# Kernel tuning notes

Measured on AMD Instinct MI355X. Metric: run time of the kernel, lower is better.

The kernel has to match this reference:

```python
import jax, jax.numpy as jnp
import numpy as np

B, T, N, F = 4, 24, 1024, 96
H, HD = 3, 32      # spatial GATConv: 3 heads, head-dim 32 (averaged -> 32 per branch, 3 branches -> 96)
GH, GHD = 4, 24    # GroupedGAT: 4 heads concatenated -> 96
E = 8192           # edges per graph


def setup_inputs() -> dict:
    key = jax.random.key(0)
    ks = jax.random.split(key, 24)
    s_in = 1.0 / np.sqrt(F)
    def gat_params(k):
        k1, k2, k3, k4 = jax.random.split(k, 4)
        return (jax.random.normal(k1, (F, H * HD), jnp.float32) * s_in,
                jax.random.normal(k2, (H, HD), jnp.float32) * 0.1,
                jax.random.normal(k3, (H, HD), jnp.float32) * 0.1,
                jax.random.normal(k4, (H, HD), jnp.float32) * 0.02)
    W_d, al_d, ar_d, b_d = gat_params(ks[3])
    W_m, al_m, ar_m, b_m = gat_params(ks[4])
    W_s, al_s, ar_s, b_s = gat_params(ks[5])
    inp = {
        "input": jax.random.normal(ks[0], (B, T, N, F), jnp.float32),
        "spatial_embedding": jax.random.normal(ks[1], (B, T, N, F), jnp.float32),
        "temporal_embedding": jax.random.normal(ks[2], (B, T, N, F), jnp.float32),
        "src_d": jax.random.randint(ks[6], (E,), 0, N, jnp.int32),
        "dst_d": (jnp.arange(E) % N).astype(jnp.int32),
        "src_m": jax.random.randint(ks[7], (E,), 0, N, jnp.int32),
        "dst_m": (jnp.arange(E) % N).astype(jnp.int32),
        "src_s": jax.random.randint(ks[8], (E,), 0, N, jnp.int32),
        "dst_s": (jnp.arange(E) % N).astype(jnp.int32),
        "W_d": W_d, "al_d": al_d, "ar_d": ar_d, "b_d": b_d,
        "W_m": W_m, "al_m": al_m, "ar_m": ar_m, "b_m": b_m,
        "W_s": W_s, "al_s": al_s, "ar_s": ar_s, "b_s": b_s,
        "Wg": jax.random.normal(ks[9], (F, GH * GHD), jnp.float32) * s_in,
        "agl": jax.random.normal(ks[10], (GH, GHD), jnp.float32) * 0.1,
        "agr": jax.random.normal(ks[11], (GH, GHD), jnp.float32) * 0.1,
        "Wf": jax.random.normal(ks[12], (2 * F, F), jnp.float32) * (1.0 / np.sqrt(2 * F)),
        "bf": jnp.zeros((F,), jnp.float32),
    }
    return inp


def _gat(x, src, dst, W, al, ar, b):
    # x: (N, K, F) node features with K = T*B batched feature slots
    K = x.shape[1]
    h = (x @ W).reshape(N, K, H, HD)                       # (N,K,H,HD)
    el = (h * al).sum(-1)                                  # (N,K,H)
    er = (h * ar).sum(-1)
    e = jax.nn.leaky_relu(el[src] + er[dst], 0.2)          # (E,K,H)
    emax = jax.ops.segment_max(e, dst, num_segments=N)
    emax = jnp.where(jnp.isfinite(emax), emax, 0.0)
    ex = jnp.exp(e - emax[dst])
    denom = jax.ops.segment_sum(ex, dst, num_segments=N)
    alpha = ex / (denom[dst] + 1e-9)                       # edge softmax over incoming edges
    out = jax.ops.segment_sum(h[src] * alpha[..., None], dst, num_segments=N)
    return (out + b).mean(2)                               # average heads -> (N,K,HD)


def reference(input, spatial_embedding, temporal_embedding,
              src_d, dst_d, src_m, dst_m, src_s, dst_s,
              W_d, al_d, ar_d, b_d, W_m, al_m, ar_m, b_m, W_s, al_s, ar_s, b_s,
              Wg, agl, agr, Wf, bf):
    # ---------------- SpatialBlock ----------------
    residual_s = input                                     # input_dim == output_dim
    x_in = input + spatial_embedding
    # torch: input.transpose(0,2).reshape(N,-1,F) -> slot order is (t,b)
    x = jnp.transpose(x_in, (2, 1, 0, 3)).reshape(N, T * B, F)
    xd = _gat(x, src_d, dst_d, W_d, al_d, ar_d, b_d)
    xm = _gat(x, src_m, dst_m, W_m, al_m, ar_m, b_m)
    xs = _gat(x, src_s, dst_s, W_s, al_s, ar_s, b_s)
    x_attn = jnp.concatenate([xd, xm, xs], axis=-1)        # (N, T*B, 3*HD=F)
    # torch: transpose(0,1).reshape(batch,T,N,-1)  (keeps original (t,b) slot order quirk)
    x_attn = jnp.transpose(x_attn, (1, 0, 2)).reshape(B, T, N, F)
    cov0 = spatial_embedding[:, 0]                         # (B,N,F)
    attn_S = jax.nn.softmax(cov0 @ jnp.swapaxes(cov0, 1, 2), axis=2)  # (B,N,N)
    # NOTE: embedding_x branch in SpatialBlock is dead code (out is overwritten); skipped.
    spatial = residual_s + x_attn

    # ---------------- TemporalBlock ----------------
    residual_t = input
    xt = jnp.swapaxes(input, 1, 2).reshape(B * N, T, F)    # (B*N, T, F), index k=b*N+n
    # GroupedGAT: dense multi-head GAT over the T=period_num time steps
    hg = (xt @ Wg).reshape(B * N, T, GH, GHD)
    elg = (hg * agl).sum(-1)                               # (BN,T,GH)
    erg = (hg * agr).sum(-1)
    eg = jax.nn.leaky_relu(elg[:, :, None, :] + erg[:, None, :, :], 0.2)  # (BN,Ti,Tj,GH)
    alphag = jax.nn.softmax(eg, axis=2)
    xg = jnp.einsum('kijh,kjhd->kihd', alphag, hg).reshape(B * N, T, GH * GHD)
    covT = temporal_embedding[:, :, 0]                     # (B,T,F)
    attn_T = jax.nn.softmax(covT @ jnp.swapaxes(covT, 1, 2), axis=1)      # softmax over dim=1 as in torch
    # torch: attn.repeat(N,1,1) paired with x of batch index b*N+n -> uses attn[(b*N+n) % B]
    idx = (jnp.arange(B * N) % B)
    emb = jnp.einsum('kij,kjf->kif', attn_T[idx], xt)      # (BN,T,F)
    xg = xg * jax.nn.sigmoid(emb)
    xg = jnp.swapaxes(xg.reshape(B, N, T, F), 1, 2)        # (B,T,N,F)
    temporal = residual_t + xg

    # ---------------- Fusion ----------------
    z = jax.nn.sigmoid(jnp.concatenate([spatial, temporal], axis=-1) @ Wf + bf)
    out = z * spatial + (1.0 - z) * temporal + input
    return out, attn_S
```

## Files before the change

### kernel.cpp

```cpp
#include <hip/hip_runtime.h>
#include <hip/hip_bf16.h>

typedef long long i64;
typedef __attribute__((ext_vector_type(8))) short short8b;
typedef __attribute__((ext_vector_type(4))) short short4b;
typedef __attribute__((ext_vector_type(4))) float f32x4;

union U8 { short8b v; ushort s[8]; };
union U4 { short4b v; ushort s[4]; };

static __device__ __forceinline__ float bs2f(ushort u) {
    union { unsigned int i; float f; } x; x.i = ((unsigned int)u) << 16; return x.f;
}
static __device__ __forceinline__ ushort f2bs(float f) {
    __hip_bfloat16 h = __float2bfloat16(f);
    return *reinterpret_cast<ushort*>(&h);
}
static __device__ __forceinline__ void mfma_bf16(f32x4& acc, short8b a, short8b b) {
    asm volatile("v_mfma_f32_16x16x32_bf16 %0, %1, %2, %0" : "+v"(acc) : "v"(a), "v"(b));
}
static __device__ __forceinline__ void mfma_fence() {
    asm volatile("s_nop 7\n\ts_nop 7\n\ts_nop 7");
}


__global__ __launch_bounds__(256) void prep_weights_kernel(
        const float* __restrict__ Wd, const float* __restrict__ Wm,
        const float* __restrict__ Ws, const float* __restrict__ Wg,
        const float* __restrict__ Wf,
        const float* __restrict__ ald, const float* __restrict__ ard,
        const float* __restrict__ alm, const float* __restrict__ arm,
        const float* __restrict__ als, const float* __restrict__ ars,
        const float* __restrict__ agl, const float* __restrict__ agr,
        ushort* __restrict__ wtab) {
    int idx = blockIdx.x * 256 + threadIdx.x;
    if (idx >= 61440) return;
    if (idx < 43008) {
        int w = idx / 10752, rem = idx - w * 10752;
        int c = rem / 96, k = rem - c * 96;
        float v;
        if (w < 3) {
            const float* W = (w == 0) ? Wd : (w == 1) ? Wm : Ws;
            if (c < 96) {
                v = W[k * 96 + c];
            } else {
                int j = c - 96, h = j >> 1;
                const float* a = (j & 1) ? ((w == 0) ? ard : (w == 1) ? arm : ars)
                                         : ((w == 0) ? ald : (w == 1) ? alm : als);
                v = 0.f;
                for (int d = 0; d < 32; ++d) v += W[k * 96 + h * 32 + d] * a[h * 32 + d];
            }
        } else {
            if (c < 96) {
                v = Wg[k * 96 + c];
            } else {
                int j = c - 96, g = j & 3;
                const float* a = (j >> 2) ? agr : agl;
                v = 0.f;
                for (int d = 0; d < 24; ++d) v += Wg[k * 96 + g * 24 + d] * a[g * 24 + d];
            }
        }
        wtab[w * 10752 + c * 96 + k] = f2bs(v);
    } else {
        int rem = idx - 43008;
        int c = rem / 192, k = rem - c * 192;
        wtab[43008 + c * 192 + k] = f2bs(Wf[k * 96 + c]);
    }
}

__global__ __launch_bounds__(256) void build_x_kernel(const float* __restrict__ inp,
                                                      const float* __restrict__ spat,
                                                      ushort* __restrict__ x) {
    int i4 = blockIdx.x * 256 + threadIdx.x;
    int q = i4 % 24;
    int r = i4 / 24;
    int n = r & 1023, bt = r >> 10;
    int t = bt % 24, b = bt / 24;
    int k = t * 4 + b;
    float4 a = ((const float4*)inp)[i4];
    float4 s = ((const float4*)spat)[i4];
    U4 u;
    u.s[0] = f2bs(a.x + s.x); u.s[1] = f2bs(a.y + s.y);
    u.s[2] = f2bs(a.z + s.z); u.s[3] = f2bs(a.w + s.w);
    *(short4b*)&x[((i64)((k << 10) | n)) * 96 + q * 4] = u.v;
}

__global__ __launch_bounds__(256) void gemm96_mfma_kernel(const ushort* __restrict__ X,
                                                          const ushort* __restrict__ wt,
                                                          ushort* __restrict__ Ho,
                                                          float* __restrict__ el,
                                                          float* __restrict__ er) {
    __shared__ ushort Xs[128 * 104];
    __shared__ ushort Wt[112 * 104];
    int tid = threadIdx.x;
    i64 row0 = (i64)blockIdx.x * 128;
    for (int i = tid; i < 1344; i += 256) {
        int c = i / 12, kg = i - c * 12;
        *(short8b*)&Wt[c * 104 + kg * 8] = *(const short8b*)&wt[c * 96 + kg * 8];
    }
    for (int i = tid; i < 1536; i += 256) {
        int r = i / 12, q = i - r * 12;
        *(short8b*)&Xs[r * 104 + q * 8] = *(const short8b*)&X[(row0 + r) * 96 + q * 8];
    }
    __syncthreads();
    int wid = tid >> 6, lane = tid & 63;
    int lr = lane & 15, lk = lane >> 4;
    f32x4 acc[2][7];
#pragma unroll
    for (int m = 0; m < 2; ++m)
#pragma unroll
        for (int c = 0; c < 7; ++c) acc[m][c] = (f32x4){0.f, 0.f, 0.f, 0.f};
    const ushort* xa = &Xs[(wid * 32 + lr) * 104 + lk * 8];
    const ushort* wb = &Wt[lr * 104 + lk * 8];
#pragma unroll
    for (int ks = 0; ks < 3; ++ks) {
        short8b a0 = *(const short8b*)(xa + ks * 32);
        short8b a1 = *(const short8b*)(xa + 16 * 104 + ks * 32);
#pragma unroll
        for (int c = 0; c < 7; ++c) {
            short8b b = *(const short8b*)(wb + c * 16 * 104 + ks * 32);
            mfma_bf16(acc[0][c], a0, b);
            mfma_bf16(acc[1][c], a1, b);
        }
    }
    mfma_fence();
#pragma unroll
    for (int m = 0; m < 2; ++m) {
#pragma unroll
        for (int c = 0; c < 6; ++c)
#pragma unroll
            for (int r = 0; r < 4; ++r) {
                i64 row = row0 + wid * 32 + m * 16 + lk * 4 + r;
                Ho[row * 96 + c * 16 + lr] = f2bs(acc[m][c][r]);
            }
        if (lr < 6) {
            float* dst = (lr & 1) ? er : el;
            int h = lr >> 1;
#pragma unroll
            for (int r = 0; r < 4; ++r) {
                i64 row = row0 + wid * 32 + m * 16 + lk * 4 + r;
                dst[row * 3 + h] = acc[m][6][r];
            }
        }
    }
}

__global__ __launch_bounds__(256) void gemm96_hg_mfma_kernel(const float* __restrict__ inp,
                                                             const ushort* __restrict__ wt,
                                                             ushort* __restrict__ Ho,
                                                             float* __restrict__ elg,
                                                             float* __restrict__ erg) {
    __shared__ ushort Xs[128 * 104];
    __shared__ ushort Wt[112 * 104];
    int tid = threadIdx.x;
    i64 row0 = (i64)blockIdx.x * 128;
    for (int i = tid; i < 1344; i += 256) {
        int c = i / 12, kg = i - c * 12;
        *(short8b*)&Wt[c * 104 + kg * 8] = *(const short8b*)&wt[c * 96 + kg * 8];
    }
    for (int i = tid; i < 3072; i += 256) {
        int r = i / 24, q = i - r * 24;
        int row = (int)row0 + r;
        int kk = row / 24, t = row - kk * 24;
        int b = kk >> 10, n = kk & 1023;
        float4 v = ((const float4*)inp)[((i64)(((b * 24 + t) << 10) | n)) * 24 + q];
        U4 u;
        u.s[0] = f2bs(v.x); u.s[1] = f2bs(v.y); u.s[2] = f2bs(v.z); u.s[3] = f2bs(v.w);
        *(short4b*)&Xs[r * 104 + q * 4] = u.v;
    }
    __syncthreads();
    int wid = tid >> 6, lane = tid & 63;
    int lr = lane & 15, lk = lane >> 4;
    f32x4 acc[2][7];
#pragma unroll
    for (int m = 0; m < 2; ++m)
#pragma unroll
        for (int c = 0; c < 7; ++c) acc[m][c] = (f32x4){0.f, 0.f, 0.f, 0.f};
    const ushort* xa = &Xs[(wid * 32 + lr) * 104 + lk * 8];
    const ushort* wb = &Wt[lr * 104 + lk * 8];
#pragma unroll
    for (int ks = 0; ks < 3; ++ks) {
        short8b a0 = *(const short8b*)(xa + ks * 32);
        short8b a1 = *(const short8b*)(xa + 16 * 104 + ks * 32);
#pragma unroll
        for (int c = 0; c < 7; ++c) {
            short8b b = *(const short8b*)(wb + c * 16 * 104 + ks * 32);
            mfma_bf16(acc[0][c], a0, b);
            mfma_bf16(acc[1][c], a1, b);
        }
    }
    mfma_fence();
#pragma unroll
    for (int m = 0; m < 2; ++m) {
#pragma unroll
        for (int c = 0; c < 6; ++c)
#pragma unroll
            for (int r = 0; r < 4; ++r) {
                i64 row = row0 + wid * 32 + m * 16 + lk * 4 + r;
                Ho[row * 96 + c * 16 + lr] = f2bs(acc[m][c][r]);
            }
        if (lr < 8) {
            float* dst = (lr >> 2) ? erg : elg;
            int g = lr & 3;
#pragma unroll
            for (int r = 0; r < 4; ++r) {
                i64 row = row0 + wid * 32 + m * 16 + lk * 4 + r;
                dst[row * 4 + g] = acc[m][6][r];
            }
        }
    }
}

__global__ __launch_bounds__(256) void gat_agg_kernel(const ushort* __restrict__ H2,
                                                      const float* __restrict__ el,
                                                      const float* __restrict__ er,
                                                      const int* __restrict__ src,
                                                      const float* __restrict__ bv,
                                                      ushort* __restrict__ xattn,
                                                      int g) {
    int tid = threadIdx.x;
    int pp = tid >> 3, l8 = tid & 7;
    int p = blockIdx.x * 32 + pp;
    int k = p >> 10, n = p & 1023;
    int d0 = l8 * 4;
    i64 kb = (i64)(k << 10);
    int s_own = src[n + l8 * 1024];
    const float* elp = &el[(kb | s_own) * 3];
    const float* erp = &er[(kb | n) * 3];
    float e[3], m[3];
#pragma unroll
    for (int h = 0; h < 3; ++h) {
        float ev = elp[h] + erp[h];
        e[h] = ev >= 0.f ? ev : 0.2f * ev;
        m[h] = e[h];
    }
#pragma unroll
    for (int mask = 1; mask < 8; mask <<= 1) {
#pragma unroll
        for (int h = 0; h < 3; ++h) m[h] = fmaxf(m[h], __shfl_xor(m[h], mask, 8));
    }
    float pex[3], S[3];
#pragma unroll
    for (int h = 0; h < 3; ++h) { pex[h] = expf(e[h] - m[h]); S[h] = pex[h]; }
#pragma unroll
    for (int mask = 1; mask < 8; mask <<= 1) {
#pragma unroll
        for (int h = 0; h < 3; ++h) S[h] += __shfl_xor(S[h], mask, 8);
    }
    float w[3];
#pragma unroll
    for (int h = 0; h < 3; ++h) w[h] = pex[h] / (S[h] + 1e-9f);
    float acc[4] = {0.f, 0.f, 0.f, 0.f};
#pragma unroll
    for (int j = 0; j < 8; ++j) {
        int sj = __shfl(s_own, j, 8);
        float a0 = __shfl(w[0], j, 8);
        float a1 = __shfl(w[1], j, 8);
        float a2 = __shfl(w[2], j, 8);
        const ushort* hp = &H2[(kb | sj) * 96 + d0];
        U4 h0, h1, h2;
        h0.v = *(const short4b*)&hp[0];
        h1.v = *(const short4b*)&hp[32];
        h2.v = *(const short4b*)&hp[64];
#pragma unroll
        for (int c = 0; c < 4; ++c)
            acc[c] += a0 * bs2f(h0.s[c]) + a1 * bs2f(h1.s[c]) + a2 * bs2f(h2.s[c]);
    }
    float4 b0 = *(const float4*)&bv[d0];
    float4 b1 = *(const float4*)&bv[32 + d0];
    float4 b2 = *(const float4*)&bv[64 + d0];
    float bsum[4] = {b0.x + b1.x + b2.x, b0.y + b1.y + b2.y,
                     b0.z + b1.z + b2.z, b0.w + b1.w + b2.w};
    U4 u;
#pragma unroll
    for (int c = 0; c < 4; ++c) u.s[c] = f2bs((acc[c] + bsum[c]) * (1.f / 3.f));
    *(short4b*)&xattn[(kb | n) * 96 + g * 32 + d0] = u.v;
}

__global__ __launch_bounds__(256) void attn_scores_kernel(const float* __restrict__ spat,
                                                          float* __restrict__ attnS) {
    int bid = blockIdx.x;
    int b = bid >> 8;
    int i0 = ((bid >> 4) & 15) * 64;
    int j0 = (bid & 15) * 64;
    const float* C = spat + (i64)b * 24 * 1024 * 96;
    __shared__ __align__(16) float As[64 * 100];
    __shared__ __align__(16) float Bs[64 * 100];
    int tid = threadIdx.x;
    float4* As4 = (float4*)As;
    float4* Bs4 = (float4*)Bs;
    const float4* Ai = (const float4*)(C + (i64)i0 * 96);
    const float4* Bj = (const float4*)(C + (i64)j0 * 96);
    for (int i = tid; i < 1536; i += 256) {
        int row = i / 24, q = i - row * 24;
        As4[row * 25 + q] = Ai[i];
        Bs4[row * 25 + q] = Bj[i];
    }
    __syncthreads();
    int tj = tid & 15, ti = tid >> 4;
    float acc[4][4];
#pragma unroll
    for (int r = 0; r < 4; ++r)
#pragma unroll
        for (int s = 0; s < 4; ++s) acc[r][s] = 0.f;
    for (int k4 = 0; k4 < 24; ++k4) {
        float4 a[4], bv[4];
#pragma unroll
        for (int r = 0; r < 4; ++r) a[r] = As4[(ti * 4 + r) * 25 + k4];
#pragma unroll
        for (int s = 0; s < 4; ++s) bv[s] = Bs4[(s * 16 + tj) * 25 + k4];
#pragma unroll
        for (int r = 0; r < 4; ++r)
#pragma unroll
            for (int s = 0; s < 4; ++s)
                acc[r][s] += a[r].x * bv[s].x + a[r].y * bv[s].y + a[r].z * bv[s].z + a[r].w * bv[s].w;
    }
#pragma unroll
    for (int r = 0; r < 4; ++r) {
        i64 orow = ((i64)(b << 10) + i0 + ti * 4 + r) * 1024 + j0;
#pragma unroll
        for (int s = 0; s < 4; ++s) attnS[orow + s * 16 + tj] = acc[r][s];
    }
}

__global__ __launch_bounds__(256) void attn_softmax_kernel(float* __restrict__ attnS) {
    i64 base = (i64)blockIdx.x * 1024;
    float4* row4 = (float4*)(attnS + base);
    int tid = threadIdx.x;
    float4 v = row4[tid];
    __shared__ float red[256];
    float m = fmaxf(fmaxf(v.x, v.y), fmaxf(v.z, v.w));
    red[tid] = m;
    __syncthreads();
    for (int st = 128; st > 0; st >>= 1) {
        if (tid < st) red[tid] = fmaxf(red[tid], red[tid + st]);
        __syncthreads();
    }
    m = red[0];
    __syncthreads();
    v.x = expf(v.x - m); v.y = expf(v.y - m); v.z = expf(v.z - m); v.w = expf(v.w - m);
    red[tid] = v.x + v.y + v.z + v.w;
    __syncthreads();
    for (int st = 128; st > 0; st >>= 1) {
        if (tid < st) red[tid] += red[tid + st];
        __syncthreads();
    }
    float inv = 1.f / red[0];
    v.x *= inv; v.y *= inv; v.z *= inv; v.w *= inv;
    row4[tid] = v;
}

__global__ __launch_bounds__(576) void attn_t_kernel(const float* __restrict__ temp,
                                                     float* __restrict__ attnT) {
    int b = blockIdx.x;
    int tid = threadIdx.x;
    __shared__ float cs[24][96];
    __shared__ float M[24][24];
    for (int i = tid; i < 2304; i += 576) {
        int r = i / 96, f = i - r * 96;
        cs[r][f] = temp[((i64)(b * 24 + r)) * 1024 * 96 + f];
    }
    __syncthreads();
    int i = tid / 24, j = tid - i * 24;
    float s = 0.f;
#pragma unroll
    for (int f = 0; f < 96; ++f) s += cs[i][f] * cs[j][f];
    M[i][j] = s;
    __syncthreads();
    float m = -1e30f;
#pragma unroll
    for (int i2 = 0; i2 < 24; ++i2) m = fmaxf(m, M[i2][j]);
    float sum = 0.f;
#pragma unroll
    for (int i2 = 0; i2 < 24; ++i2) sum += expf(M[i2][j] - m);
    attnT[((i64)b * 24 + i) * 24 + j] = expf(M[i][j] - m) / sum;
}

__global__ __launch_bounds__(192) void temporal_kernel(const float* __restrict__ inp,
                                                       const ushort* __restrict__ hg,
                                                       const float* __restrict__ elgb,
                                                       const float* __restrict__ ergb,
                                                       const float* __restrict__ attnT,
                                                       ushort* __restrict__ gated) {
    int kk = blockIdx.x;
    int b = kk >> 10, n = kk & 1023;
    __shared__ __align__(16) ushort hgs[24 * 96];
    __shared__ __align__(16) ushort xs[24 * 96];
    __shared__ __align__(16) float alphaT[4][24][32];
    __shared__ __align__(16) float atT[24][32];
    __shared__ __align__(16) float elg[24][4], erg[24][4];
    int tid = threadIdx.x;
    for (int i = tid; i < 576; i += 192)
        *(short4b*)&hgs[i * 4] = *(const short4b*)&hg[(i64)kk * 2304 + i * 4];
    for (int i = tid; i < 576; i += 192) {
        int r = i / 24, q = i - r * 24;
        float4 v = ((const float4*)inp)[(((i64)(b * 24 + r)) << 10 | n) * 24 + q];
        U4 u;
        u.s[0] = f2bs(v.x); u.s[1] = f2bs(v.y); u.s[2] = f2bs(v.z); u.s[3] = f2bs(v.w);
        *(short4b*)&xs[r * 96 + q * 4] = u.v;
    }
    int ib = kk & 3;
    for (int i = tid; i < 576; i += 192) {
        int ii = i / 24, j = i - ii * 24;
        atT[j][(ii / 3) * 4 + (ii - (ii / 3) * 3)] = attnT[ib * 576 + i];
    }
    for (int i = tid; i < 48; i += 192) {
        int r = i >> 1;
        if (i & 1) *(float4*)&erg[r][0] = ((const float4*)ergb)[(i64)kk * 24 + r];
        else       *(float4*)&elg[r][0] = ((const float4*)elgb)[(i64)kk * 24 + r];
    }
    __syncthreads();
    {
        int i = tid >> 3, g = (tid >> 1) & 3, half = tid & 1;
        int j0 = half * 12;
        float eli = elg[i][g];
        float ev[12];
        float m = -1e30f;
#pragma unroll
        for (int j = 0; j < 12; ++j) {
            float e = eli + erg[j0 + j][g];
            e = e >= 0.f ? e : 0.2f * e;
            ev[j] = e;
            m = fmaxf(m, e);
        }
        m = fmaxf(m, __shfl_xor(m, 1));
        float sum = 0.f;
#pragma unroll
        for (int j = 0; j < 12; ++j) { ev[j] = expf(ev[j] - m); sum += ev[j]; }
        sum += __shfl_xor(sum, 1);
        float inv = 1.f / sum;
        int slot = (i / 3) * 4 + (i - (i / 3) * 3);
#pragma unroll
        for (int j = 0; j < 12; ++j) alphaT[g][j0 + j][slot] = ev[j] * inv;
    }
    __syncthreads();
    int ig = tid / 24, f4 = tid - (tid / 24) * 24;
    int g = f4 / 6;
    float4 xg0 = {0,0,0,0}, xg1 = {0,0,0,0}, xg2 = {0,0,0,0};
    float4 em0 = {0,0,0,0}, em1 = {0,0,0,0}, em2 = {0,0,0,0};
#pragma unroll
    for (int j = 0; j < 24; ++j) {
        U4 uh, ux;
        uh.v = *(const short4b*)&hgs[j * 96 + f4 * 4];
        ux.v = *(const short4b*)&xs[j * 96 + f4 * 4];
        float4 a4 = *(const float4*)&alphaT[g][j][ig * 4];
        float4 w4 = *(const float4*)&atT[j][ig * 4];
        float h0 = bs2f(uh.s[0]), h1 = bs2f(uh.s[1]), h2 = bs2f(uh.s[2]), h3 = bs2f(uh.s[3]);
        float x0 = bs2f(ux.s[0]), x1 = bs2f(ux.s[1]), x2 = bs2f(ux.s[2]), x3 = bs2f(ux.s[3]);
        xg0.x += a4.x * h0; xg0.y += a4.x * h1; xg0.z += a4.x * h2; xg0.w += a4.x * h3;
        xg1.x += a4.y * h0; xg1.y += a4.y * h1; xg1.z += a4.y * h2; xg1.w += a4.y * h3;
        xg2.x += a4.z * h0; xg2.y += a4.z * h1; xg2.z += a4.z * h2; xg2.w += a4.z * h3;
        em0.x += w4.x * x0; em0.y += w4.x * x1; em0.z += w4.x * x2; em0.w += w4.x * x3;
        em1.x += w4.y * x0; em1.y += w4.y * x1; em1.z += w4.y * x2; em1.w += w4.y * x3;
        em2.x += w4.z * x0; em2.y += w4.z * x1; em2.z += w4.z * x2; em2.w += w4.z * x3;
    }
    i64 obase = (i64)kk * 2304 + f4 * 4;
#pragma unroll
    for (int r = 0; r < 3; ++r) {
        float4 xg = (r == 0) ? xg0 : (r == 1) ? xg1 : xg2;
        float4 em = (r == 0) ? em0 : (r == 1) ? em1 : em2;
        U4 o;
        o.s[0] = f2bs(xg.x / (1.f + expf(-em.x)));
        o.s[1] = f2bs(xg.y / (1.f + expf(-em.y)));
        o.s[2] = f2bs(xg.z / (1.f + expf(-em.z)));
        o.s[3] = f2bs(xg.w / (1.f + expf(-em.w)));
        *(short4b*)&gated[obase + (i64)(ig * 3 + r) * 96] = o.v;
    }
}

__global__ __launch_bounds__(256) void fusion_mfma_kernel(const float* __restrict__ inp,
                                                          const ushort* __restrict__ xattn,
                                                          const ushort* __restrict__ gated,
                                                          const ushort* __restrict__ wtf,
                                                          const float* __restrict__ bfv,
                                                          float* __restrict__ outb) {
    __shared__ ushort Xs[64 * 200];
    __shared__ ushort Wt[96 * 200];
    int tid = threadIdx.x;
    i64 row0 = (i64)blockIdx.x * 64;
    for (int i = tid; i < 2304; i += 256) {
        int c = i / 24, kg = i - c * 24;
        *(short8b*)&Wt[c * 200 + kg * 8] = *(const short8b*)&wtf[c * 192 + kg * 8];
    }
    for (int i = tid; i < 768; i += 256) {
        int r = i / 12, q = i - r * 12;
        i64 grow = row0 + r;
        int n = (int)(grow & 1023);
        int bt = (int)(grow >> 10);
        int t = bt % 24, b = bt / 24;
        float4 iv0 = ((const float4*)inp)[grow * 24 + q * 2];
        float4 iv1 = ((const float4*)inp)[grow * 24 + q * 2 + 1];
        U8 xa; xa.v = *(const short8b*)&xattn[grow * 96 + q * 8];
        U8 gd; gd.v = *(const short8b*)&gated[(((i64)((b << 10) | n)) * 24 + t) * 96 + q * 8];
        float ivf[8] = {iv0.x, iv0.y, iv0.z, iv0.w, iv1.x, iv1.y, iv1.z, iv1.w};
        U8 sp, tm;
#pragma unroll
        for (int j = 0; j < 8; ++j) {
            sp.s[j] = f2bs(ivf[j] + bs2f(xa.s[j]));
            tm.s[j] = f2bs(ivf[j] + bs2f(gd.s[j]));
        }
        *(short8b*)&Xs[r * 200 + q * 8] = sp.v;
        *(short8b*)&Xs[r * 200 + 96 + q * 8] = tm.v;
    }
    __syncthreads();
    int wid = tid >> 6, lane = tid & 63;
    int lr = lane & 15, lk = lane >> 4;
    f32x4 acc[6];
#pragma unroll
    for (int c = 0; c < 6; ++c) acc[c] = (f32x4){0.f, 0.f, 0.f, 0.f};
    const ushort* xa = &Xs[(wid * 16 + lr) * 200 + lk * 8];
    const ushort* wb = &Wt[lr * 200 + lk * 8];
#pragma unroll
    for (int ks = 0; ks < 6; ++ks) {
        short8b a = *(const short8b*)(xa + ks * 32);
#pragma unroll
        for (int c = 0; c < 6; ++c) {
            short8b b = *(const short8b*)(wb + c * 16 * 200 + ks * 32);
            mfma_bf16(acc[c], a, b);
        }
    }
    mfma_fence();
#pragma unroll
    for (int c = 0; c < 6; ++c) {
        int col = c * 16 + lr;
        float bfc = bfv[col];
#pragma unroll
        for (int r = 0; r < 4; ++r) {
            int lrow = wid * 16 + lk * 4 + r;
            i64 grow = row0 + lrow;
            float z = 1.f / (1.f + expf(-(acc[c][r] + bfc)));
            float sp = bs2f(Xs[lrow * 200 + col]);
            float tm = bs2f(Xs[lrow * 200 + 96 + col]);
            float iv = inp[grow * 96 + col];
            outb[grow * 96 + col] = z * sp + (1.f - z) * tm + iv;
        }
    }
}

extern "C" void kernel_launch(void* const* d_in, const int* in_sizes, int n_in,
                              void* d_out, int out_size, void* d_ws, size_t ws_size,
                              hipStream_t stream) {
    const float* input = (const float*)d_in[0];
    const float* spat  = (const float*)d_in[1];
    const float* temp  = (const float*)d_in[2];
    const int* src_d = (const int*)d_in[3];
    const int* src_m = (const int*)d_in[5];
    const int* src_s = (const int*)d_in[7];
    const float* W_d  = (const float*)d_in[9];
    const float* al_d = (const float*)d_in[10];
    const float* ar_d = (const float*)d_in[11];
    const float* b_d  = (const float*)d_in[12];
    const float* W_m  = (const float*)d_in[13];
    const float* al_m = (const float*)d_in[14];
    const float* ar_m = (const float*)d_in[15];
    const float* b_m  = (const float*)d_in[16];
    const float* W_s  = (const float*)d_in[17];
    const float* al_s = (const float*)d_in[18];
    const float* ar_s = (const float*)d_in[19];
    const float* b_s  = (const float*)d_in[20];
    const float* Wg   = (const float*)d_in[21];
    const float* agl  = (const float*)d_in[22];
    const float* agr  = (const float*)d_in[23];
    const float* Wf   = (const float*)d_in[24];
    const float* bf_  = (const float*)d_in[25];

    float* outb  = (float*)d_out;
    float* attnS = outb + 9437184;

    float* wsf = (float*)d_ws;
    ushort* xbf      = (ushort*)wsf;
    ushort* hgbf     = xbf;
    ushort* H2bf     = (ushort*)(wsf + 4718592);
    ushort* gatedbf  = H2bf;
    ushort* xattnbf  = (ushort*)(wsf + 9437184);
    float* el    = wsf + 14155776;
    float* er    = el + 294912;
    float* elgb  = wsf + 14155776;
    float* attnT = wsf + 14745600;
    float* ergb  = wsf + 14747904;
    ushort* wtab = (ushort*)(wsf + 15141120);
    ushort* wt_d = wtab;
    ushort* wt_m = wtab + 10752;
    ushort* wt_s = wtab + 21504;
    ushort* wtg  = wtab + 32256;
    ushort* wtf  = wtab + 43008;

    prep_weights_kernel<<<240, 256, 0, stream>>>(W_d, W_m, W_s, Wg, Wf,
                                                 al_d, ar_d, al_m, ar_m, al_s, ar_s,
                                                 agl, agr, wtab);
    build_x_kernel<<<9216, 256, 0, stream>>>(input, spat, xbf);

    const ushort* Wgat[3] = {wt_d, wt_m, wt_s};
    const float* bgat[3] = {b_d, b_m, b_s};
    const int* srcs[3] = {src_d, src_m, src_s};
    for (int g = 0; g < 3; ++g) {
        gemm96_mfma_kernel<<<768, 256, 0, stream>>>(xbf, Wgat[g], H2bf, el, er);
        gat_agg_kernel<<<3072, 256, 0, stream>>>(H2bf, el, er, srcs[g], bgat[g],
                                                 xattnbf, g);
    }

    attn_scores_kernel<<<1024, 256, 0, stream>>>(spat, attnS);
    attn_softmax_kernel<<<4096, 256, 0, stream>>>(attnS);

    gemm96_hg_mfma_kernel<<<768, 256, 0, stream>>>(input, wtg, hgbf, elgb, ergb);
    attn_t_kernel<<<4, 576, 0, stream>>>(temp, attnT);
    temporal_kernel<<<4096, 192, 0, stream>>>(input, hgbf, elgb, ergb, attnT, gatedbf);
    fusion_mfma_kernel<<<1536, 256, 0, stream>>>(input, xattnbf, gatedbf, wtf, bf_, outb);
}
```

Before: 245.1 us.

## Split temporal kernel into sigmoid-embedding and grouped-GAT aggregation kernels

Splits the fused temporal kernel in two. A new 576-thread kernel computes sigmoid(attn_T @ x) in fp32 and writes it as bf16 into the output buffer, used as scratch. The aggregation kernel then only computes the grouped-GAT weighted sum and multiplies by the precomputed sigmoid, with an XOR swizzle on the alpha shared-memory layout to reduce bank conflicts. The goal is lower register and LDS pressure per kernel, bought with an extra 18MB bf16 round trip through global memory and one more launch.

```diff
diff --git a/kernel.cpp b/kernel.cpp
--- a/kernel.cpp
+++ b/kernel.cpp
@@ -376,34 +376,50 @@
     attnT[((i64)b * 24 + i) * 24 + j] = expf(M[i][j] - m) / sum;
 }
 
-__global__ __launch_bounds__(192) void temporal_kernel(const float* __restrict__ inp,
-                                                       const ushort* __restrict__ hg,
-                                                       const float* __restrict__ elgb,
-                                                       const float* __restrict__ ergb,
-                                                       const float* __restrict__ attnT,
-                                                       ushort* __restrict__ gated) {
+__global__ __launch_bounds__(576) void sig_kernel(const float* __restrict__ inp,
+                                                  const float* __restrict__ attnT,
+                                                  ushort* __restrict__ sig) {
     int kk = blockIdx.x;
     int b = kk >> 10, n = kk & 1023;
+    __shared__ __align__(16) float xs[24 * 100];
+    __shared__ float ats[576];
+    int tid = threadIdx.x;
+    {
+        int r = tid / 24, q = tid - (tid / 24) * 24;
+        *(float4*)&xs[r * 100 + q * 4] =
+            ((const float4*)inp)[(((i64)(b * 24 + r)) << 10 | n) * 24 + q];
+        ats[tid] = attnT[(kk & 3) * 576 + tid];
+    }
+    __syncthreads();
+    int i = tid / 24, f4 = tid - (tid / 24) * 24;
+    const float* ap = &ats[i * 24];
+    float4 acc = {0.f, 0.f, 0.f, 0.f};
+#pragma unroll
+    for (int j = 0; j < 24; ++j) {
+        float a = ap[j];
+        float4 v = *(const float4*)&xs[j * 100 + f4 * 4];
+        acc.x += a * v.x; acc.y += a * v.y; acc.z += a * v.z; acc.w += a * v.w;
+    }
+    U4 o;
+    o.s[0] = f2bs(1.f / (1.f + expf(-acc.x)));
+    o.s[1] = f2bs(1.f / (1.f + expf(-acc.y)));
+    o.s[2] = f2bs(1.f / (1.f + expf(-acc.z)));
+    o.s[3] = f2bs(1.f / (1.f + expf(-acc.w)));
+    *(short4b*)&sig[(i64)kk * 2304 + i * 96 + f4 * 4] = o.v;
+}
+
+__global__ __launch_bounds__(192) void xg_kernel(const ushort* __restrict__ hg,
+                                                 const float* __restrict__ elgb,
+                                                 const float* __restrict__ ergb,
+                                                 const ushort* __restrict__ sig,
+                                                 ushort* __restrict__ gated) {
+    int kk = blockIdx.x;
     __shared__ __align__(16) ushort hgs[24 * 96];
-    __shared__ __align__(16) ushort xs[24 * 96];
-    __shared__ __align__(16) float alphaT[4][24][32];
-    __shared__ __align__(16) float atT[24][32];
+    __shared__ __align__(16) float alphaT[4 * 24 * 32];
     __shared__ __align__(16) float elg[24][4], erg[24][4];
     int tid = threadIdx.x;
     for (int i = tid; i < 576; i += 192)
         *(short4b*)&hgs[i * 4] = *(const short4b*)&hg[(i64)kk * 2304 + i * 4];
-    for (int i = tid; i < 576; i += 192) {
-        int r = i / 24, q = i - r * 24;
-        float4 v = ((const float4*)inp)[(((i64)(b * 24 + r)) << 10 | n) * 24 + q];
-        U4 u;
-        u.s[0] = f2bs(v.x); u.s[1] = f2bs(v.y); u.s[2] = f2bs(v.z); u.s[3] = f2bs(v.w);
-        *(short4b*)&xs[r * 96 + q * 4] = u.v;
-    }
-    int ib = kk & 3;
-    for (int i = tid; i < 576; i += 192) {
-        int ii = i / 24, j = i - ii * 24;
-        atT[j][(ii / 3) * 4 + (ii - (ii / 3) * 3)] = attnT[ib * 576 + i];
-    }
     for (int i = tid; i < 48; i += 192) {
         int r = i >> 1;
         if (i & 1) *(float4*)&erg[r][0] = ((const float4*)ergb)[(i64)kk * 24 + r];
@@ -429,42 +445,36 @@
         for (int j = 0; j < 12; ++j) { ev[j] = expf(ev[j] - m); sum += ev[j]; }
         sum += __shfl_xor(sum, 1);
         float inv = 1.f / sum;
-        int slot = (i / 3) * 4 + (i - (i / 3) * 3);
-#pragma unroll
-        for (int j = 0; j < 12; ++j) alphaT[g][j0 + j][slot] = ev[j] * inv;
+        int slot = ((i / 3) * 4 + (i - (i / 3) * 3)) ^ (g << 3);
+#pragma unroll
+        for (int j = 0; j < 12; ++j) alphaT[g * 768 + (j0 + j) * 32 + slot] = ev[j] * inv;
     }
     __syncthreads();
     int ig = tid / 24, f4 = tid - (tid / 24) * 24;
     int g = f4 / 6;
     float4 xg0 = {0,0,0,0}, xg1 = {0,0,0,0}, xg2 = {0,0,0,0};
-    float4 em0 = {0,0,0,0}, em1 = {0,0,0,0}, em2 = {0,0,0,0};
+    const float* aT = &alphaT[g * 768 + ((ig * 4) ^ (g << 3))];
 #pragma unroll
     for (int j = 0; j < 24; ++j) {
-        U4 uh, ux;
-        uh.v = *(const short4b*)&hgs[j * 96 + f4 * 4];
-        ux.v = *(const short4b*)&xs[j * 96 + f4 * 4];
-        float4 a4 = *(const float4*)&alphaT[g][j][ig * 4];
-        float4 w4 = *(const float4*)&atT[j][ig * 4];
+        U4 uh; uh.v = *(const short4b*)&hgs[j * 96 + f4 * 4];
+        float4 a4 = *(const float4*)&aT[j * 32];
         float h0 = bs2f(uh.s[0]), h1 = bs2f(uh.s[1]), h2 = bs2f(uh.s[2]), h3 = bs2f(uh.s[3]);
-        float x0 = bs2f(ux.s[0]), x1 = bs2f(ux.s[1]), x2 = bs2f(ux.s[2]), x3 = bs2f(ux.s[3]);
         xg0.x += a4.x * h0; xg0.y += a4.x * h1; xg0.z += a4.x * h2; xg0.w += a4.x * h3;
         xg1.x += a4.y * h0; xg1.y += a4.y * h1; xg1.z += a4.y * h2; xg1.w += a4.y * h3;
         xg2.x += a4.z * h0; xg2.y += a4.z * h1; xg2.z += a4.z * h2; xg2.w += a4.z * h3;
-        em0.x += w4.x * x0; em0.y += w4.x * x1; em0.z += w4.x * x2; em0.w += w4.x * x3;
-        em1.x += w4.y * x0; em1.y += w4.y * x1; em1.z += w4.y * x2; em1.w += w4.y * x3;
-        em2.x += w4.z * x0; em2.y += w4.z * x1; em2.z += w4.z * x2; em2.w += w4.z * x3;
     }
     i64 obase = (i64)kk * 2304 + f4 * 4;
 #pragma unroll
     for (int r = 0; r < 3; ++r) {
         float4 xg = (r == 0) ? xg0 : (r == 1) ? xg1 : xg2;
-        float4 em = (r == 0) ? em0 : (r == 1) ? em1 : em2;
+        i64 off = obase + (i64)(ig * 3 + r) * 96;
+        U4 us; us.v = *(const short4b*)&sig[off];
         U4 o;
-        o.s[0] = f2bs(xg.x / (1.f + expf(-em.x)));
-        o.s[1] = f2bs(xg.y / (1.f + expf(-em.y)));
-        o.s[2] = f2bs(xg.z / (1.f + expf(-em.z)));
-        o.s[3] = f2bs(xg.w / (1.f + expf(-em.w)));
-        *(short4b*)&gated[obase + (i64)(ig * 3 + r) * 96] = o.v;
+        o.s[0] = f2bs(xg.x * bs2f(us.s[0]));
+        o.s[1] = f2bs(xg.y * bs2f(us.s[1]));
+        o.s[2] = f2bs(xg.z * bs2f(us.s[2]));
+        o.s[3] = f2bs(xg.w * bs2f(us.s[3]));
+        *(short4b*)&gated[off] = o.v;
     }
 }
 
@@ -584,6 +594,7 @@
     ushort* wt_s = wtab + 21504;
     ushort* wtg  = wtab + 32256;
     ushort* wtf  = wtab + 43008;
+    ushort* sigbf = (ushort*)outb;
 
     prep_weights_kernel<<<240, 256, 0, stream>>>(W_d, W_m, W_s, Wg, Wf,
                                                  al_d, ar_d, al_m, ar_m, al_s, ar_s,
@@ -602,8 +613,9 @@
     attn_scores_kernel<<<1024, 256, 0, stream>>>(spat, attnS);
     attn_softmax_kernel<<<4096, 256, 0, stream>>>(attnS);
 
+    attn_t_kernel<<<4, 576, 0, stream>>>(temp, attnT);
+    sig_kernel<<<4096, 576, 0, stream>>>(input, attnT, sigbf);
     gemm96_hg_mfma_kernel<<<768, 256, 0, stream>>>(input, wtg, hgbf, elgb, ergb);
-    attn_t_kernel<<<4, 576, 0, stream>>>(temp, attnT);
-    temporal_kernel<<<4096, 192, 0, stream>>>(input, hgbf, elgb, ergb, attnT, gatedbf);
+    xg_kernel<<<4096, 192, 0, stream>>>(hgbf, elgb, ergb, sigbf, gatedbf);
     fusion_mfma_kernel<<<1536, 256, 0, stream>>>(input, xattnbf, gatedbf, wtf, bf_, outb);
 }
```

Measured after the change: 244.5 us. About the same (-0.2%).
